# Optimization experiments

Hardware: AMD Instinct MI355X
Metric: run time of the kernel (lower is better)

The kernel has to match this reference:

```python
import jax, jax.numpy as jnp
import numpy as np

B, N_O, N_Q = 2, 512, 512
POS_DIM, LATENT, HEADS, HEAD_DIM, OUT_DIM = 3, 256, 8, 32, 128
HD = HEADS * HEAD_DIM  # == LATENT here


def _lin(key, fan_in, fan_out):
    return jax.random.normal(key, (fan_in, fan_out), jnp.float32) / np.sqrt(fan_in)


def setup_inputs() -> dict:
    key = jax.random.key(0)
    ks = jax.random.split(key, 12)
    return {
        'h_obs': jax.random.normal(ks[0], (B, N_O, LATENT), jnp.float32),
        'pos_obs': jax.random.uniform(ks[1], (B, N_O, POS_DIM), jnp.float32),
        'pos_query': jax.random.uniform(ks[2], (B, N_Q, POS_DIM), jnp.float32),
        'fw1': _lin(ks[3], LATENT, LATENT), 'fb1': jnp.zeros((LATENT,), jnp.float32),
        'fw2': _lin(ks[4], LATENT, HD), 'fb2': jnp.zeros((HD,), jnp.float32),
        'log_sigma': jnp.zeros((HEADS,), jnp.float32),
        'kw1': _lin(ks[5], POS_DIM * 3, LATENT), 'kb1': jnp.zeros((LATENT,), jnp.float32),
        'kw2': _lin(ks[6], LATENT, HEADS), 'kb2': jnp.zeros((HEADS,), jnp.float32),
        'ow': _lin(ks[7], HD, OUT_DIM), 'ob': jnp.zeros((OUT_DIM,), jnp.float32),
        'vw': _lin(ks[8], HD, OUT_DIM), 'vb': jnp.zeros((OUT_DIM,), jnp.float32),
    }


def reference(h_obs, pos_obs, pos_query, fw1, fb1, fw2, fb2, log_sigma,
              kw1, kb1, kw2, kb2, ow, ob, vw, vb):
    Bv, No, _ = h_obs.shape
    Nq = pos_query.shape[1]
    # feature net -> values [B, H, N_o, D]
    v = jax.nn.relu(h_obs @ fw1 + fb1) @ fw2 + fb2
    v = v.reshape(Bv, No, HEADS, HEAD_DIM).transpose(0, 2, 1, 3)
    # pairwise relative positions [B, Nq, No, P]
    pos_q = pos_query[:, :, None, :]
    pos_o = pos_obs[:, None, :, :]
    rel = pos_q - pos_o
    dist2 = jnp.sum(rel ** 2, axis=-1)  # [B, Nq, No]
    sigma = jnp.exp(log_sigma)[None, :, None, None]
    rbf = jnp.exp(-dist2[:, None] / (sigma ** 2 + 1e-6))  # [B, H, Nq, No]
    # kernel MLP on concatenated pairwise positions [B, Nq, No, 3P] -> [B, H, Nq, No]
    ki = jnp.concatenate([
        jnp.broadcast_to(pos_q, (Bv, Nq, No, POS_DIM)),
        jnp.broadcast_to(pos_o, (Bv, Nq, No, POS_DIM)),
        rel], axis=-1)
    delta = (jax.nn.relu(ki @ kw1 + kb1) @ kw2 + kb2).transpose(0, 3, 1, 2)
    logits = jnp.log(rbf + 1e-8) + delta
    weights = jax.nn.softmax(logits, axis=-1)  # [B, H, Nq, No]
    # weighted mean over observations
    v_mean = jnp.einsum('bhqo,bhod->bhqd', weights, v)  # [B, H, Nq, D]
    h_query = v_mean.transpose(0, 2, 1, 3).reshape(Bv, Nq, HD)
    # weighted variance: sum_o w * (v_o - v_mean)^2
    residual = v[:, :, None, :, :] - v_mean[:, :, :, None, :]  # [B, H, Nq, No, D]
    var = jnp.sum(weights[..., None] * residual ** 2, axis=3)  # [B, H, Nq, D]
    var = var.transpose(0, 2, 1, 3).reshape(Bv, Nq, HD)
    mean = h_query @ ow + ob
    var_out = jax.nn.softplus(var @ vw + vb)
    return (mean, var_out)
```

## Files before the change

### kernel.cpp

```cpp
#include <hip/hip_runtime.h>
#include <math.h>

#define NB 2
#define NO 512
#define NQ 512
#define OUT_DIM 128
#define LPAD 516

typedef __attribute__((ext_vector_type(8))) short short8;
typedef __attribute__((ext_vector_type(4))) float f32x4;
typedef float v2f __attribute__((ext_vector_type(2)));

__device__ __forceinline__ float softplus_f(float x) {
  return x > 0.0f ? x + log1pf(expf(-x)) : log1pf(expf(x));
}
__device__ __forceinline__ unsigned short bf16_rne(float f) {
  unsigned u = __float_as_uint(f);
  unsigned r = u + 0x7FFFu + ((u >> 16) & 1u);
  return (unsigned short)(r >> 16);
}
__device__ __forceinline__ float bf16_to_f32(unsigned short h) {
  return __uint_as_float(((unsigned)h) << 16);
}

#if defined(__has_builtin)
#if __has_builtin(__builtin_amdgcn_cvt_pk_bf16_f32)
#define HAS_CVT_PK_BF16 1
#endif
#endif

__device__ __forceinline__ unsigned pack_bf2(float x, float y) {
#ifdef HAS_CVT_PK_BF16
  auto r = __builtin_amdgcn_cvt_pk_bf16_f32(x, y);
  unsigned u; __builtin_memcpy(&u, &r, 4);
  return u;
#else
  unsigned ux = __float_as_uint(x);
  unsigned uy = __float_as_uint(y);
  ux = ux + 0x7FFFu + ((ux >> 16) & 1u);
  uy = uy + 0x7FFFu + ((uy >> 16) & 1u);
  return (ux >> 16) | (uy & 0xFFFF0000u);
#endif
}
__device__ __forceinline__ v2f unpk_bf2(unsigned u) {
  v2f r; r.x = __uint_as_float(u << 16); r.y = __uint_as_float(u & 0xFFFF0000u);
  return r;
}
__device__ __forceinline__ v2f splat2(float x) { v2f r; r.x = x; r.y = x; return r; }
__device__ __forceinline__ v2f fma2(v2f a, v2f b, v2f c) { return __builtin_elementwise_fma(a, b, c); }
__device__ __forceinline__ v2f max2(v2f a, v2f b) { return __builtin_elementwise_max(a, b); }

__global__ __launch_bounds__(512) void prep_kernel(
    const float* __restrict__ h_obs, const float* __restrict__ fw1,
    const float* __restrict__ fb1, const float* __restrict__ fw2,
    const float* __restrict__ fb2, const float* __restrict__ pos_obs,
    const float* __restrict__ kw1, unsigned short* __restrict__ V_bf,
    unsigned short* __restrict__ AO_bf)
{
  if (blockIdx.x < 512) {
    __shared__ float s_red[2][2][256];
    __shared__ float s_hid[2][256];
    const int n  = threadIdx.x & 255;
    const int ks = threadIdx.x >> 8;
    const int r0 = blockIdx.x * 2;
    const int k0 = ks * 128;
    float a0 = 0.f, a1 = 0.f;
    #pragma unroll 8
    for (int kk = 0; kk < 128; ++kk) {
      int k = k0 + kk;
      float w = fw1[k * 256 + n];
      a0 = fmaf(h_obs[(r0 + 0) * 256 + k], w, a0);
      a1 = fmaf(h_obs[(r0 + 1) * 256 + k], w, a1);
    }
    s_red[ks][0][n] = a0; s_red[ks][1][n] = a1;
    __syncthreads();
    if (ks == 0) {
      float bb = fb1[n];
      s_hid[0][n] = fmaxf(s_red[0][0][n] + s_red[1][0][n] + bb, 0.f);
      s_hid[1][n] = fmaxf(s_red[0][1][n] + s_red[1][1][n] + bb, 0.f);
    }
    __syncthreads();
    float c0 = 0.f, c1 = 0.f;
    #pragma unroll 8
    for (int kk = 0; kk < 128; ++kk) {
      int k = k0 + kk;
      float w = fw2[k * 256 + n];
      c0 = fmaf(s_hid[0][k], w, c0);
      c1 = fmaf(s_hid[1][k], w, c1);
    }
    __syncthreads();
    s_red[ks][0][n] = c0; s_red[ks][1][n] = c1;
    __syncthreads();
    if (ks == 0) {
      float bb = fb2[n];
      V_bf[(size_t)(r0 + 0) * 256 + n] = bf16_rne(s_red[0][0][n] + s_red[1][0][n] + bb);
      V_bf[(size_t)(r0 + 1) * 256 + n] = bf16_rne(s_red[0][1][n] + s_red[1][1][n] + bb);
    }
  } else {
    const int i     = blockIdx.x - 512;
    const int b     = i >> 8;
    const int chunk = i & 255;
    const int ol    = threadIdx.x >> 8;
    const int j     = threadIdx.x & 255;
    const int o     = chunk * 2 + ol;
    float c0 = kw1[3 * 256 + j] - kw1[6 * 256 + j];
    float c1 = kw1[4 * 256 + j] - kw1[7 * 256 + j];
    float c2 = kw1[5 * 256 + j] - kw1[8 * 256 + j];
    const float* p = pos_obs + ((size_t)(b * NO + o)) * 3;
    AO_bf[(size_t)(b * NO + o) * 256 + j] =
        bf16_rne(fmaf(p[0], c0, fmaf(p[1], c1, p[2] * c2)));
  }
}

__global__ __launch_bounds__(512, 6) void attn_fused(
    const unsigned short* __restrict__ V_bf,
    const unsigned short* __restrict__ AO_bf,
    const float* __restrict__ kw1,
    const float* __restrict__ kb1,
    const float* __restrict__ kw2,
    const float* __restrict__ kb2,
    const float* __restrict__ log_sigma,
    const float* __restrict__ pos_obs,
    const float* __restrict__ pos_query,
    const float* __restrict__ ow, const float* __restrict__ obias,
    const float* __restrict__ vw, const float* __restrict__ vbias,
    float* __restrict__ out)
{
  __shared__ float s_logits[2][8 * LPAD];
  __shared__ __align__(16) char poolA[16512];
  __shared__ __align__(16) char poolB[4096];
  __shared__ float s_sum[2][8];
  __shared__ float s_invs2[8];
  __shared__ float s_kb2v[8];

  short8* Bhi    = (short8*)poolA;
  short8* Blo    = (short8*)(poolA + 8192);
  float*  s_redC = (float*)poolA;
  float*  s_pred = (float*)poolA;
  float*  s_aq   = (float*)poolB;
  float*  s_hv   = (float*)poolB;

  const int t   = threadIdx.x;
  const int bq0 = blockIdx.x * 2;
  const int b   = bq0 >> 9;

  float pqx[2], pqy[2], pqz[2];
  #pragma unroll
  for (int q = 0; q < 2; ++q) {
    pqx[q] = pos_query[(bq0 + q) * 3 + 0];
    pqy[q] = pos_query[(bq0 + q) * 3 + 1];
    pqz[q] = pos_query[(bq0 + q) * 3 + 2];
  }
  {
    const int q = t >> 8, j = t & 255;
    float c0 = kw1[0 * 256 + j] + kw1[6 * 256 + j];
    float c1 = kw1[1 * 256 + j] + kw1[7 * 256 + j];
    float c2 = kw1[2 * 256 + j] + kw1[8 * 256 + j];
    s_aq[q * 256 + j] =
        fmaf(pqx[q], c0, fmaf(pqy[q], c1, fmaf(pqz[q], c2, kb1[j])));
  }
  {
    const int kstep = t >> 6, lane = t & 63;
    const int nh = lane & 15;
    const int kb_ = kstep * 32 + ((lane >> 4) & 3) * 8;
    short8 hi8, lo8;
    #pragma unroll
    for (int i = 0; i < 8; ++i) {
      float v = (nh < 8) ? kw2[(kb_ + i) * 8 + nh] : 0.f;
      unsigned short h = bf16_rne(v);
      hi8[i] = (short)h;
      lo8[i] = (short)bf16_rne(v - bf16_to_f32(h));
    }
    Bhi[kstep * 64 + lane] = hi8;
    Blo[kstep * 64 + lane] = lo8;
  }
  if (t < 8) {
    float s = expf(log_sigma[t]);
    s_invs2[t] = 1.0f / (s * s + 1e-6f);
    s_kb2v[t]  = kb2[t];
  }
  __syncthreads();

  {
    const int o = t;
    const float* p = pos_obs + (size_t)(b * NO + o) * 3;
    float px = p[0], py = p[1], pz = p[2];
    float d2q[2];
    #pragma unroll
    for (int q = 0; q < 2; ++q) {
      float r0 = pqx[q] - px, r1 = pqy[q] - py, r2 = pqz[q] - pz;
      d2q[q] = r0 * r0 + r1 * r1 + r2 * r2;
    }
    #pragma unroll
    for (int h = 0; h < 8; ++h) {
      float inv = s_invs2[h];
      float kbv = s_kb2v[h];
      s_logits[0][h * LPAD + o] = logf(expf(-d2q[0] * inv) + 1e-8f) + kbv;
      s_logits[1][h * LPAD + o] = logf(expf(-d2q[1] * inv) + 1e-8f) + kbv;
    }
  }

  {
    const int wave = t >> 6, lane = t & 63;
    const int quad = lane >> 4, mrow = lane & 15;
    const int tb   = wave * 4;
    f32x4 C[2][4];
    #pragma unroll
    for (int q = 0; q < 2; ++q)
      #pragma unroll
      for (int jt = 0; jt < 4; ++jt) C[q][jt] = (f32x4){0.f, 0.f, 0.f, 0.f};

    for (int kstep = 0; kstep < 8; ++kstep) {
      const int koff = kstep * 32 + quad * 8;
      const v2f* aqp0 = (const v2f*)(s_aq + koff);
      const v2f* aqp1 = (const v2f*)(s_aq + 256 + koff);
      v2f aq0[4], aq1[4];
      #pragma unroll
      for (int i = 0; i < 4; ++i) { aq0[i] = aqp0[i]; aq1[i] = aqp1[i]; }
      short8 bhi = Bhi[kstep * 64 + lane];
      short8 blo = Blo[kstep * 64 + lane];
      #pragma unroll
      for (int jt = 0; jt < 4; ++jt) {
        const int o = (tb + jt) * 16 + mrow;
        int4 u = *(const int4*)(AO_bf + ((size_t)(b * NO + o) << 8) + koff);
        v2f ao[4];
        ao[0] = unpk_bf2((unsigned)u.x); ao[1] = unpk_bf2((unsigned)u.y);
        ao[2] = unpk_bf2((unsigned)u.z); ao[3] = unpk_bf2((unsigned)u.w);
        v2f z = splat2(0.f);
        int4 af0, af1;
        {
          v2f h0 = max2(aq0[0] + ao[0], z), h1 = max2(aq0[1] + ao[1], z);
          v2f h2 = max2(aq0[2] + ao[2], z), h3 = max2(aq0[3] + ao[3], z);
          af0.x = (int)pack_bf2(h0.x, h0.y); af0.y = (int)pack_bf2(h1.x, h1.y);
          af0.z = (int)pack_bf2(h2.x, h2.y); af0.w = (int)pack_bf2(h3.x, h3.y);
        }
        {
          v2f h0 = max2(aq1[0] + ao[0], z), h1 = max2(aq1[1] + ao[1], z);
          v2f h2 = max2(aq1[2] + ao[2], z), h3 = max2(aq1[3] + ao[3], z);
          af1.x = (int)pack_bf2(h0.x, h0.y); af1.y = (int)pack_bf2(h1.x, h1.y);
          af1.z = (int)pack_bf2(h2.x, h2.y); af1.w = (int)pack_bf2(h3.x, h3.y);
        }
        short8 a0 = __builtin_bit_cast(short8, af0);
        short8 a1 = __builtin_bit_cast(short8, af1);
        C[0][jt] = __builtin_amdgcn_mfma_f32_16x16x32_bf16(a0, bhi, C[0][jt], 0, 0, 0);
        C[0][jt] = __builtin_amdgcn_mfma_f32_16x16x32_bf16(a0, blo, C[0][jt], 0, 0, 0);
        C[1][jt] = __builtin_amdgcn_mfma_f32_16x16x32_bf16(a1, bhi, C[1][jt], 0, 0, 0);
        C[1][jt] = __builtin_amdgcn_mfma_f32_16x16x32_bf16(a1, blo, C[1][jt], 0, 0, 0);
      }
    }
    __syncthreads();

    const int h = lane & 15;
    if (h < 8) {
      #pragma unroll
      for (int q = 0; q < 2; ++q)
        #pragma unroll
        for (int jt = 0; jt < 4; ++jt) {
          const int ob = (tb + jt) * 16 + quad * 4;
          #pragma unroll
          for (int r = 0; r < 4; ++r)
            s_logits[q][h * LPAD + ob + r] += C[q][jt][r];
        }
    }
  }
  __syncthreads();

  {
    const int wave = t >> 6, lane = t & 63;
    #pragma unroll
    for (int cc = 0; cc < 2; ++cc) {
      const int c = wave * 2 + cc;
      const int q = c >> 3, h = c & 7;
      float* pl = &s_logits[q][h * LPAD];
      float l[8];
      float m = -1e30f;
      #pragma unroll
      for (int k = 0; k < 8; ++k) {
        l[k] = pl[k * 64 + lane];
        m = fmaxf(m, l[k]);
      }
      #pragma unroll
      for (int off = 32; off >= 1; off >>= 1) m = fmaxf(m, __shfl_xor(m, off, 64));
      float s = 0.f;
      #pragma unroll
      for (int k = 0; k < 8; ++k) {
        float p = expf(l[k] - m);
        pl[k * 64 + lane] = p;
        s += p;
      }
      #pragma unroll
      for (int off = 32; off >= 1; off >>= 1) s += __shfl_xor(s, off, 64);
      if (lane == 0) s_sum[q][h] = s;
    }
  }
  __syncthreads();

  float q1p[8];
  {
    const int s  = t >> 6;
    const int r  = t & 63;
    const int h  = r >> 3, dg = r & 7;
    const unsigned short* vb_ = V_bf + ((size_t)(b * NO) << 8) + h * 32 + dg * 4;
    const float* P0 = &s_logits[0][h * LPAD + s * 64];
    const float* P1 = &s_logits[1][h * LPAD + s * 64];
    v2f s1a0 = splat2(0.f), s1b0 = splat2(0.f), s2a0 = splat2(0.f), s2b0 = splat2(0.f);
    v2f s1a1 = splat2(0.f), s1b1 = splat2(0.f), s2a1 = splat2(0.f), s2b1 = splat2(0.f);
    const int o0 = s * 64;
    #pragma unroll 2
    for (int oi = 0; oi < 64; oi += 4) {
      float4 pv0 = *(const float4*)&P0[oi];
      float4 pv1 = *(const float4*)&P1[oi];
      #pragma unroll
      for (int i = 0; i < 4; ++i) {
        const int o = o0 + oi + i;
        uint2 vv = *(const uint2*)(vb_ + ((size_t)o << 8));
        v2f va  = unpk_bf2(vv.x);
        v2f vb2 = unpk_bf2(vv.y);
        v2f p0 = splat2((&pv0.x)[i]), p1 = splat2((&pv1.x)[i]);
        s1a0 = fma2(p0, va, s1a0);  s1b0 = fma2(p0, vb2, s1b0);
        v2f t0a = p0 * va, t0b = p0 * vb2;
        s2a0 = fma2(t0a, va, s2a0); s2b0 = fma2(t0b, vb2, s2b0);
        s1a1 = fma2(p1, va, s1a1);  s1b1 = fma2(p1, vb2, s1b1);
        v2f t1a = p1 * va, t1b = p1 * vb2;
        s2a1 = fma2(t1a, va, s2a1); s2b1 = fma2(t1b, vb2, s2b1);
      }
    }
    s_redC[0 * LPAD + t] = s1a0.x; s_redC[1 * LPAD + t] = s1a0.y;
    s_redC[2 * LPAD + t] = s1b0.x; s_redC[3 * LPAD + t] = s1b0.y;
    s_redC[4 * LPAD + t] = s2a0.x; s_redC[5 * LPAD + t] = s2a0.y;
    s_redC[6 * LPAD + t] = s2b0.x; s_redC[7 * LPAD + t] = s2b0.y;
    q1p[0] = s1a1.x; q1p[1] = s1a1.y; q1p[2] = s1b1.x; q1p[3] = s1b1.y;
    q1p[4] = s2a1.x; q1p[5] = s2a1.y; q1p[6] = s2b1.x; q1p[7] = s2b1.y;
  }
  __syncthreads();
  if (t < 256) {
    const int hd = t, h = hd >> 5, d = hd & 31, dg = d >> 2, c = d & 3;
    float S1 = 0.f, S2 = 0.f;
    #pragma unroll
    for (int s = 0; s < 8; ++s) {
      const int idx = s * 64 + h * 8 + dg;
      S1 += s_redC[c * LPAD + idx];
      S2 += s_redC[(4 + c) * LPAD + idx];
    }
    float inv = 1.0f / s_sum[0][h];
    float m1 = S1 * inv;
    float va = fmaxf(S2 * inv - m1 * m1, 0.f);
    s_hv[0 * 256 + hd] = m1;
    s_hv[1 * 256 + hd] = va;
  }
  __syncthreads();
  {
    #pragma unroll
    for (int i = 0; i < 8; ++i) s_redC[i * LPAD + t] = q1p[i];
  }
  __syncthreads();
  if (t < 256) {
    const int hd = t, h = hd >> 5, d = hd & 31, dg = d >> 2, c = d & 3;
    float S1 = 0.f, S2 = 0.f;
    #pragma unroll
    for (int s = 0; s < 8; ++s) {
      const int idx = s * 64 + h * 8 + dg;
      S1 += s_redC[c * LPAD + idx];
      S2 += s_redC[(4 + c) * LPAD + idx];
    }
    float inv = 1.0f / s_sum[1][h];
    float m1 = S1 * inv;
    float va = fmaxf(S2 * inv - m1 * m1, 0.f);
    s_hv[2 * 256 + hd] = m1;
    s_hv[3 * 256 + hd] = va;
  }
  __syncthreads();

  {
    const int ks = t >> 8, mode = (t >> 7) & 1, n = t & 127;
    const float* W  = mode ? vw : ow;
    const float* X0 = s_hv + mode * 256;
    const float* X1 = s_hv + (2 + mode) * 256;
    float a0 = 0.f, a1 = 0.f;
    const int k0 = ks * 128;
    #pragma unroll 4
    for (int k = k0; k < k0 + 128; k += 4) {
      float4 x0 = *(const float4*)&X0[k];
      float4 x1 = *(const float4*)&X1[k];
      float w0 = W[(k + 0) * 128 + n];
      float w1 = W[(k + 1) * 128 + n];
      float w2 = W[(k + 2) * 128 + n];
      float w3 = W[(k + 3) * 128 + n];
      a0 = fmaf(x0.x, w0, a0); a1 = fmaf(x1.x, w0, a1);
      a0 = fmaf(x0.y, w1, a0); a1 = fmaf(x1.y, w1, a1);
      a0 = fmaf(x0.z, w2, a0); a1 = fmaf(x1.z, w2, a1);
      a0 = fmaf(x0.w, w3, a0); a1 = fmaf(x1.w, w3, a1);
    }
    s_pred[((ks * 2 + mode) * 2 + 0) * 128 + n] = a0;
    s_pred[((ks * 2 + mode) * 2 + 1) * 128 + n] = a1;
  }
  __syncthreads();
  {
    const int q = t >> 8, mode = (t >> 7) & 1, n = t & 127;
    float v = s_pred[((0 * 2 + mode) * 2 + q) * 128 + n]
            + s_pred[((1 * 2 + mode) * 2 + q) * 128 + n]
            + (mode ? vbias[n] : obias[n]);
    if (mode) v = softplus_f(v);
    out[(size_t)mode * (NB * NQ * OUT_DIM) + (size_t)(bq0 + q) * OUT_DIM + n] = v;
  }
}

extern "C" void kernel_launch(void* const* d_in, const int* in_sizes, int n_in,
                              void* d_out, int out_size, void* d_ws, size_t ws_size,
                              hipStream_t stream)
{
  const float* h_obs     = (const float*)d_in[0];
  const float* pos_obs   = (const float*)d_in[1];
  const float* pos_query = (const float*)d_in[2];
  const float* fw1       = (const float*)d_in[3];
  const float* fb1       = (const float*)d_in[4];
  const float* fw2       = (const float*)d_in[5];
  const float* fb2       = (const float*)d_in[6];
  const float* log_sigma = (const float*)d_in[7];
  const float* kw1       = (const float*)d_in[8];
  const float* kb1       = (const float*)d_in[9];
  const float* kw2       = (const float*)d_in[10];
  const float* kb2       = (const float*)d_in[11];
  const float* ow        = (const float*)d_in[12];
  const float* ob        = (const float*)d_in[13];
  const float* vw        = (const float*)d_in[14];
  const float* vb        = (const float*)d_in[15];

  float* out = (float*)d_out;
  unsigned short* ws = (unsigned short*)d_ws;

  unsigned short* V_bf  = ws;
  unsigned short* AO_bf = ws + 262144;

  prep_kernel<<<1024, 512, 0, stream>>>(h_obs, fw1, fb1, fw2, fb2,
                                        pos_obs, kw1, V_bf, AO_bf);
  attn_fused<<<NB * NQ / 2, 512, 0, stream>>>(V_bf, AO_bf, kw1, kb1, kw2, kb2,
                                              log_sigma, pos_obs, pos_query,
                                              ow, ob, vw, vb, out);
}
```

Before: 154.2 us.

## Process one query per block with 256 threads instead of two queries per 512-thread block

Restructures the fused attention kernel so each block handles a single query with 256 threads, launching 1024 blocks instead of 512. Shared memory per block roughly halves and register pressure per thread drops, aiming for more resident blocks and better latency hiding. The cost is giving up reuse across two queries: each AO tile and V row is now loaded and unpacked once per query rather than once per pair, and the kw2 split and output weights are reloaded per query.

New measurement: 164.6 us. 1.07x slower.

```diff
diff --git a/kernel.cpp b/kernel.cpp
--- a/kernel.cpp
+++ b/kernel.cpp
@@ -6,6 +6,7 @@
 #define NQ 512
 #define OUT_DIM 128
 #define LPAD 516
+#define RPITCH 260
 
 typedef __attribute__((ext_vector_type(8))) short short8;
 typedef __attribute__((ext_vector_type(4))) float f32x4;
@@ -112,7 +113,7 @@
   }
 }
 
-__global__ __launch_bounds__(512, 6) void attn_fused(
+__global__ __launch_bounds__(256, 4) void attn_fused(
     const unsigned short* __restrict__ V_bf,
     const unsigned short* __restrict__ AO_bf,
     const float* __restrict__ kw1,
@@ -126,53 +127,51 @@
     const float* __restrict__ vw, const float* __restrict__ vbias,
     float* __restrict__ out)
 {
-  __shared__ float s_logits[2][8 * LPAD];
-  __shared__ __align__(16) char poolA[16512];
-  __shared__ __align__(16) char poolB[4096];
-  __shared__ float s_sum[2][8];
+  __shared__ float s_logits[8 * LPAD];
+  __shared__ __align__(16) char poolA[16384];
+  __shared__ __align__(16) char poolB[2048];
+  __shared__ float s_sum[8];
   __shared__ float s_invs2[8];
   __shared__ float s_kb2v[8];
 
   short8* Bhi    = (short8*)poolA;
   short8* Blo    = (short8*)(poolA + 8192);
   float*  s_redC = (float*)poolA;
-  float*  s_pred = (float*)poolA;
   float*  s_aq   = (float*)poolB;
   float*  s_hv   = (float*)poolB;
 
-  const int t   = threadIdx.x;
-  const int bq0 = blockIdx.x * 2;
-  const int b   = bq0 >> 9;
-
-  float pqx[2], pqy[2], pqz[2];
-  #pragma unroll
-  for (int q = 0; q < 2; ++q) {
-    pqx[q] = pos_query[(bq0 + q) * 3 + 0];
-    pqy[q] = pos_query[(bq0 + q) * 3 + 1];
-    pqz[q] = pos_query[(bq0 + q) * 3 + 2];
-  }
-  {
-    const int q = t >> 8, j = t & 255;
+  const int t  = threadIdx.x;
+  const int bq = blockIdx.x;
+  const int b  = bq >> 9;
+
+  const float pqx = pos_query[bq * 3 + 0];
+  const float pqy = pos_query[bq * 3 + 1];
+  const float pqz = pos_query[bq * 3 + 2];
+  {
+    const int j = t;
     float c0 = kw1[0 * 256 + j] + kw1[6 * 256 + j];
     float c1 = kw1[1 * 256 + j] + kw1[7 * 256 + j];
     float c2 = kw1[2 * 256 + j] + kw1[8 * 256 + j];
-    s_aq[q * 256 + j] =
-        fmaf(pqx[q], c0, fmaf(pqy[q], c1, fmaf(pqz[q], c2, kb1[j])));
-  }
-  {
-    const int kstep = t >> 6, lane = t & 63;
+    s_aq[j] = fmaf(pqx, c0, fmaf(pqy, c1, fmaf(pqz, c2, kb1[j])));
+  }
+  {
+    const int lane = t & 63;
     const int nh = lane & 15;
-    const int kb_ = kstep * 32 + ((lane >> 4) & 3) * 8;
-    short8 hi8, lo8;
-    #pragma unroll
-    for (int i = 0; i < 8; ++i) {
-      float v = (nh < 8) ? kw2[(kb_ + i) * 8 + nh] : 0.f;
-      unsigned short h = bf16_rne(v);
-      hi8[i] = (short)h;
-      lo8[i] = (short)bf16_rne(v - bf16_to_f32(h));
-    }
-    Bhi[kstep * 64 + lane] = hi8;
-    Blo[kstep * 64 + lane] = lo8;
+    #pragma unroll
+    for (int kk = 0; kk < 2; ++kk) {
+      const int kstep = (t >> 6) + kk * 4;
+      const int kb_ = kstep * 32 + ((lane >> 4) & 3) * 8;
+      short8 hi8, lo8;
+      #pragma unroll
+      for (int i = 0; i < 8; ++i) {
+        float v = (nh < 8) ? kw2[(kb_ + i) * 8 + nh] : 0.f;
+        unsigned short h = bf16_rne(v);
+        hi8[i] = (short)h;
+        lo8[i] = (short)bf16_rne(v - bf16_to_f32(h));
+      }
+      Bhi[kstep * 64 + lane] = hi8;
+      Blo[kstep * 64 + lane] = lo8;
+    }
   }
   if (t < 8) {
     float s = expf(log_sigma[t]);
@@ -181,71 +180,48 @@
   }
   __syncthreads();
 
-  {
-    const int o = t;
+  #pragma unroll
+  for (int oo = 0; oo < 2; ++oo) {
+    const int o = t + oo * 256;
     const float* p = pos_obs + (size_t)(b * NO + o) * 3;
-    float px = p[0], py = p[1], pz = p[2];
-    float d2q[2];
-    #pragma unroll
-    for (int q = 0; q < 2; ++q) {
-      float r0 = pqx[q] - px, r1 = pqy[q] - py, r2 = pqz[q] - pz;
-      d2q[q] = r0 * r0 + r1 * r1 + r2 * r2;
-    }
-    #pragma unroll
-    for (int h = 0; h < 8; ++h) {
-      float inv = s_invs2[h];
-      float kbv = s_kb2v[h];
-      s_logits[0][h * LPAD + o] = logf(expf(-d2q[0] * inv) + 1e-8f) + kbv;
-      s_logits[1][h * LPAD + o] = logf(expf(-d2q[1] * inv) + 1e-8f) + kbv;
-    }
+    float r0 = pqx - p[0], r1 = pqy - p[1], r2 = pqz - p[2];
+    float d2 = r0 * r0 + r1 * r1 + r2 * r2;
+    #pragma unroll
+    for (int h = 0; h < 8; ++h)
+      s_logits[h * LPAD + o] = logf(expf(-d2 * s_invs2[h]) + 1e-8f) + s_kb2v[h];
   }
 
   {
     const int wave = t >> 6, lane = t & 63;
     const int quad = lane >> 4, mrow = lane & 15;
-    const int tb   = wave * 4;
-    f32x4 C[2][4];
-    #pragma unroll
-    for (int q = 0; q < 2; ++q)
-      #pragma unroll
-      for (int jt = 0; jt < 4; ++jt) C[q][jt] = (f32x4){0.f, 0.f, 0.f, 0.f};
+    const int tb   = wave * 8;
+    f32x4 C[8];
+    #pragma unroll
+    for (int jt = 0; jt < 8; ++jt) C[jt] = (f32x4){0.f, 0.f, 0.f, 0.f};
 
     for (int kstep = 0; kstep < 8; ++kstep) {
       const int koff = kstep * 32 + quad * 8;
-      const v2f* aqp0 = (const v2f*)(s_aq + koff);
-      const v2f* aqp1 = (const v2f*)(s_aq + 256 + koff);
-      v2f aq0[4], aq1[4];
-      #pragma unroll
-      for (int i = 0; i < 4; ++i) { aq0[i] = aqp0[i]; aq1[i] = aqp1[i]; }
+      const v2f* aqp = (const v2f*)(s_aq + koff);
+      v2f aq[4];
+      #pragma unroll
+      for (int i = 0; i < 4; ++i) aq[i] = aqp[i];
       short8 bhi = Bhi[kstep * 64 + lane];
       short8 blo = Blo[kstep * 64 + lane];
-      #pragma unroll
-      for (int jt = 0; jt < 4; ++jt) {
+      #pragma unroll 4
+      for (int jt = 0; jt < 8; ++jt) {
         const int o = (tb + jt) * 16 + mrow;
         int4 u = *(const int4*)(AO_bf + ((size_t)(b * NO + o) << 8) + koff);
-        v2f ao[4];
-        ao[0] = unpk_bf2((unsigned)u.x); ao[1] = unpk_bf2((unsigned)u.y);
-        ao[2] = unpk_bf2((unsigned)u.z); ao[3] = unpk_bf2((unsigned)u.w);
         v2f z = splat2(0.f);
-        int4 af0, af1;
-        {
-          v2f h0 = max2(aq0[0] + ao[0], z), h1 = max2(aq0[1] + ao[1], z);
-          v2f h2 = max2(aq0[2] + ao[2], z), h3 = max2(aq0[3] + ao[3], z);
-          af0.x = (int)pack_bf2(h0.x, h0.y); af0.y = (int)pack_bf2(h1.x, h1.y);
-          af0.z = (int)pack_bf2(h2.x, h2.y); af0.w = (int)pack_bf2(h3.x, h3.y);
-        }
-        {
-          v2f h0 = max2(aq1[0] + ao[0], z), h1 = max2(aq1[1] + ao[1], z);
-          v2f h2 = max2(aq1[2] + ao[2], z), h3 = max2(aq1[3] + ao[3], z);
-          af1.x = (int)pack_bf2(h0.x, h0.y); af1.y = (int)pack_bf2(h1.x, h1.y);
-          af1.z = (int)pack_bf2(h2.x, h2.y); af1.w = (int)pack_bf2(h3.x, h3.y);
-        }
-        short8 a0 = __builtin_bit_cast(short8, af0);
-        short8 a1 = __builtin_bit_cast(short8, af1);
-        C[0][jt] = __builtin_amdgcn_mfma_f32_16x16x32_bf16(a0, bhi, C[0][jt], 0, 0, 0);
-        C[0][jt] = __builtin_amdgcn_mfma_f32_16x16x32_bf16(a0, blo, C[0][jt], 0, 0, 0);
-        C[1][jt] = __builtin_amdgcn_mfma_f32_16x16x32_bf16(a1, bhi, C[1][jt], 0, 0, 0);
-        C[1][jt] = __builtin_amdgcn_mfma_f32_16x16x32_bf16(a1, blo, C[1][jt], 0, 0, 0);
+        v2f h0 = max2(aq[0] + unpk_bf2((unsigned)u.x), z);
+        v2f h1 = max2(aq[1] + unpk_bf2((unsigned)u.y), z);
+        v2f h2 = max2(aq[2] + unpk_bf2((unsigned)u.z), z);
+        v2f h3 = max2(aq[3] + unpk_bf2((unsigned)u.w), z);
+        int4 af;
+        af.x = (int)pack_bf2(h0.x, h0.y); af.y = (int)pack_bf2(h1.x, h1.y);
+        af.z = (int)pack_bf2(h2.x, h2.y); af.w = (int)pack_bf2(h3.x, h3.y);
+        short8 a = __builtin_bit_cast(short8, af);
+        C[jt] = __builtin_amdgcn_mfma_f32_16x16x32_bf16(a, bhi, C[jt], 0, 0, 0);
+        C[jt] = __builtin_amdgcn_mfma_f32_16x16x32_bf16(a, blo, C[jt], 0, 0, 0);
       }
     }
     __syncthreads();
@@ -253,14 +229,12 @@
     const int h = lane & 15;
     if (h < 8) {
       #pragma unroll
-      for (int q = 0; q < 2; ++q)
+      for (int jt = 0; jt < 8; ++jt) {
+        const int ob = (tb + jt) * 16 + quad * 4;
         #pragma unroll
-        for (int jt = 0; jt < 4; ++jt) {
-          const int ob = (tb + jt) * 16 + quad * 4;
-          #pragma unroll
-          for (int r = 0; r < 4; ++r)
-            s_logits[q][h * LPAD + ob + r] += C[q][jt][r];
-        }
+        for (int r = 0; r < 4; ++r)
+          s_logits[h * LPAD + ob + r] += C[jt][r];
+      }
     }
   }
   __syncthreads();
@@ -269,9 +243,8 @@
     const int wave = t >> 6, lane = t & 63;
     #pragma unroll
     for (int cc = 0; cc < 2; ++cc) {
-      const int c = wave * 2 + cc;
-      const int q = c >> 3, h = c & 7;
-      float* pl = &s_logits[q][h * LPAD];
+      const int h = wave * 2 + cc;
+      float* pl = &s_logits[h * LPAD];
       float l[8];
       float m = -1e30f;
       #pragma unroll
@@ -290,118 +263,75 @@
       }
       #pragma unroll
       for (int off = 32; off >= 1; off >>= 1) s += __shfl_xor(s, off, 64);
-      if (lane == 0) s_sum[q][h] = s;
-    }
-  }
-  __syncthreads();
-
-  float q1p[8];
+      if (lane == 0) s_sum[h] = s;
+    }
+  }
+  __syncthreads();
+
   {
     const int s  = t >> 6;
     const int r  = t & 63;
     const int h  = r >> 3, dg = r & 7;
     const unsigned short* vb_ = V_bf + ((size_t)(b * NO) << 8) + h * 32 + dg * 4;
-    const float* P0 = &s_logits[0][h * LPAD + s * 64];
-    const float* P1 = &s_logits[1][h * LPAD + s * 64];
-    v2f s1a0 = splat2(0.f), s1b0 = splat2(0.f), s2a0 = splat2(0.f), s2b0 = splat2(0.f);
-    v2f s1a1 = splat2(0.f), s1b1 = splat2(0.f), s2a1 = splat2(0.f), s2b1 = splat2(0.f);
-    const int o0 = s * 64;
+    const float* P = &s_logits[h * LPAD + s * 128];
+    v2f s1a = splat2(0.f), s1b = splat2(0.f), s2a = splat2(0.f), s2b = splat2(0.f);
+    const int o0 = s * 128;
     #pragma unroll 2
-    for (int oi = 0; oi < 64; oi += 4) {
-      float4 pv0 = *(const float4*)&P0[oi];
-      float4 pv1 = *(const float4*)&P1[oi];
+    for (int oi = 0; oi < 128; oi += 4) {
+      float4 pv = *(const float4*)&P[oi];
       #pragma unroll
       for (int i = 0; i < 4; ++i) {
         const int o = o0 + oi + i;
         uint2 vv = *(const uint2*)(vb_ + ((size_t)o << 8));
         v2f va  = unpk_bf2(vv.x);
         v2f vb2 = unpk_bf2(vv.y);
-        v2f p0 = splat2((&pv0.x)[i]), p1 = splat2((&pv1.x)[i]);
-        s1a0 = fma2(p0, va, s1a0);  s1b0 = fma2(p0, vb2, s1b0);
-        v2f t0a = p0 * va, t0b = p0 * vb2;
-        s2a0 = fma2(t0a, va, s2a0); s2b0 = fma2(t0b, vb2, s2b0);
-        s1a1 = fma2(p1, va, s1a1);  s1b1 = fma2(p1, vb2, s1b1);
-        v2f t1a = p1 * va, t1b = p1 * vb2;
-        s2a1 = fma2(t1a, va, s2a1); s2b1 = fma2(t1b, vb2, s2b1);
-      }
-    }
-    s_redC[0 * LPAD + t] = s1a0.x; s_redC[1 * LPAD + t] = s1a0.y;
-    s_redC[2 * LPAD + t] = s1b0.x; s_redC[3 * LPAD + t] = s1b0.y;
-    s_redC[4 * LPAD + t] = s2a0.x; s_redC[5 * LPAD + t] = s2a0.y;
-    s_redC[6 * LPAD + t] = s2b0.x; s_redC[7 * LPAD + t] = s2b0.y;
-    q1p[0] = s1a1.x; q1p[1] = s1a1.y; q1p[2] = s1b1.x; q1p[3] = s1b1.y;
-    q1p[4] = s2a1.x; q1p[5] = s2a1.y; q1p[6] = s2b1.x; q1p[7] = s2b1.y;
-  }
-  __syncthreads();
-  if (t < 256) {
+        v2f p = splat2((&pv.x)[i]);
+        s1a = fma2(p, va, s1a);  s1b = fma2(p, vb2, s1b);
+        v2f ta = p * va, tb = p * vb2;
+        s2a = fma2(ta, va, s2a); s2b = fma2(tb, vb2, s2b);
+      }
+    }
+    __syncthreads();
+    s_redC[0 * RPITCH + t] = s1a.x; s_redC[1 * RPITCH + t] = s1a.y;
+    s_redC[2 * RPITCH + t] = s1b.x; s_redC[3 * RPITCH + t] = s1b.y;
+    s_redC[4 * RPITCH + t] = s2a.x; s_redC[5 * RPITCH + t] = s2a.y;
+    s_redC[6 * RPITCH + t] = s2b.x; s_redC[7 * RPITCH + t] = s2b.y;
+  }
+  __syncthreads();
+
+  {
     const int hd = t, h = hd >> 5, d = hd & 31, dg = d >> 2, c = d & 3;
     float S1 = 0.f, S2 = 0.f;
     #pragma unroll
-    for (int s = 0; s < 8; ++s) {
+    for (int s = 0; s < 4; ++s) {
       const int idx = s * 64 + h * 8 + dg;
-      S1 += s_redC[c * LPAD + idx];
-      S2 += s_redC[(4 + c) * LPAD + idx];
-    }
-    float inv = 1.0f / s_sum[0][h];
+      S1 += s_redC[c * RPITCH + idx];
+      S2 += s_redC[(4 + c) * RPITCH + idx];
+    }
+    float inv = 1.0f / s_sum[h];
     float m1 = S1 * inv;
     float va = fmaxf(S2 * inv - m1 * m1, 0.f);
+    __syncthreads();
     s_hv[0 * 256 + hd] = m1;
     s_hv[1 * 256 + hd] = va;
   }
   __syncthreads();
-  {
-    #pragma unroll
-    for (int i = 0; i < 8; ++i) s_redC[i * LPAD + t] = q1p[i];
-  }
-  __syncthreads();
-  if (t < 256) {
-    const int hd = t, h = hd >> 5, d = hd & 31, dg = d >> 2, c = d & 3;
-    float S1 = 0.f, S2 = 0.f;
-    #pragma unroll
-    for (int s = 0; s < 8; ++s) {
-      const int idx = s * 64 + h * 8 + dg;
-      S1 += s_redC[c * LPAD + idx];
-      S2 += s_redC[(4 + c) * LPAD + idx];
-    }
-    float inv = 1.0f / s_sum[1][h];
-    float m1 = S1 * inv;
-    float va = fmaxf(S2 * inv - m1 * m1, 0.f);
-    s_hv[2 * 256 + hd] = m1;
-    s_hv[3 * 256 + hd] = va;
-  }
-  __syncthreads();
-
-  {
-    const int ks = t >> 8, mode = (t >> 7) & 1, n = t & 127;
+
+  {
+    const int mode = t >> 7, n = t & 127;
     const float* W  = mode ? vw : ow;
-    const float* X0 = s_hv + mode * 256;
-    const float* X1 = s_hv + (2 + mode) * 256;
-    float a0 = 0.f, a1 = 0.f;
-    const int k0 = ks * 128;
+    const float* X  = s_hv + mode * 256;
+    float acc = mode ? vbias[n] : obias[n];
     #pragma unroll 4
-    for (int k = k0; k < k0 + 128; k += 4) {
-      float4 x0 = *(const float4*)&X0[k];
-      float4 x1 = *(const float4*)&X1[k];
-      float w0 = W[(k + 0) * 128 + n];
-      float w1 = W[(k + 1) * 128 + n];
-      float w2 = W[(k + 2) * 128 + n];
-      float w3 = W[(k + 3) * 128 + n];
-      a0 = fmaf(x0.x, w0, a0); a1 = fmaf(x1.x, w0, a1);
-      a0 = fmaf(x0.y, w1, a0); a1 = fmaf(x1.y, w1, a1);
-      a0 = fmaf(x0.z, w2, a0); a1 = fmaf(x1.z, w2, a1);
-      a0 = fmaf(x0.w, w3, a0); a1 = fmaf(x1.w, w3, a1);
-    }
-    s_pred[((ks * 2 + mode) * 2 + 0) * 128 + n] = a0;
-    s_pred[((ks * 2 + mode) * 2 + 1) * 128 + n] = a1;
-  }
-  __syncthreads();
-  {
-    const int q = t >> 8, mode = (t >> 7) & 1, n = t & 127;
-    float v = s_pred[((0 * 2 + mode) * 2 + q) * 128 + n]
-            + s_pred[((1 * 2 + mode) * 2 + q) * 128 + n]
-            + (mode ? vbias[n] : obias[n]);
-    if (mode) v = softplus_f(v);
-    out[(size_t)mode * (NB * NQ * OUT_DIM) + (size_t)(bq0 + q) * OUT_DIM + n] = v;
+    for (int k = 0; k < 256; k += 4) {
+      float4 x = *(const float4*)&X[k];
+      acc = fmaf(x.x, W[(k + 0) * 128 + n], acc);
+      acc = fmaf(x.y, W[(k + 1) * 128 + n], acc);
+      acc = fmaf(x.z, W[(k + 2) * 128 + n], acc);
+      acc = fmaf(x.w, W[(k + 3) * 128 + n], acc);
+    }
+    if (mode) acc = softplus_f(acc);
+    out[(size_t)mode * (NB * NQ * OUT_DIM) + (size_t)bq * OUT_DIM + n] = acc;
   }
 }
 
@@ -434,7 +364,7 @@
 
   prep_kernel<<<1024, 512, 0, stream>>>(h_obs, fw1, fb1, fw2, fb2,
                                         pos_obs, kw1, V_bf, AO_bf);
-  attn_fused<<<NB * NQ / 2, 512, 0, stream>>>(V_bf, AO_bf, kw1, kb1, kw2, kb2,
-                                              log_sigma, pos_obs, pos_query,
-                                              ow, ob, vw, vb, out);
-}
+  attn_fused<<<NB * NQ, 256, 0, stream>>>(V_bf, AO_bf, kw1, kb1, kw2, kb2,
+                                          log_sigma, pos_obs, pos_query,
+                                          ow, ob, vw, vb, out);
+}
```

## Fuse RBF logits into MFMA epilogue and restructure value reduction per query

Applied to the files above, without the earlier changes.

The RBF log-term computation moves out of its separate pass: squared distances are precomputed into shared memory and the log/exp term is added in the MFMA epilogue, which removes one sync and a read-modify-write of the logits. The weighted mean/variance loop now assigns each thread one query with 8 dims via 16-byte loads instead of two queries with 4 dims. This doubles the shared reduction buffer so both queries reduce in one pass, dropping two barriers. Fast __expf/__logf intrinsics replace expf/logf/log1pf, and the occupancy hint is dropped, at some accuracy and LDS-occupancy risk.

Measured after the change: 159.8 us. 1.04x slower.

```diff
diff --git a/kernel.cpp b/kernel.cpp
--- a/kernel.cpp
+++ b/kernel.cpp
@@ -6,13 +6,14 @@
 #define NQ 512
 #define OUT_DIM 128
 #define LPAD 516
+#define RP2  516
 
 typedef __attribute__((ext_vector_type(8))) short short8;
 typedef __attribute__((ext_vector_type(4))) float f32x4;
 typedef float v2f __attribute__((ext_vector_type(2)));
 
 __device__ __forceinline__ float softplus_f(float x) {
-  return x > 0.0f ? x + log1pf(expf(-x)) : log1pf(expf(x));
+  return x > 0.0f ? x + __logf(1.0f + __expf(-x)) : __logf(1.0f + __expf(x));
 }
 __device__ __forceinline__ unsigned short bf16_rne(float f) {
   unsigned u = __float_as_uint(f);
@@ -112,7 +113,7 @@
   }
 }
 
-__global__ __launch_bounds__(512, 6) void attn_fused(
+__global__ __launch_bounds__(512) void attn_fused(
     const unsigned short* __restrict__ V_bf,
     const unsigned short* __restrict__ AO_bf,
     const float* __restrict__ kw1,
@@ -127,8 +128,8 @@
     float* __restrict__ out)
 {
   __shared__ float s_logits[2][8 * LPAD];
-  __shared__ __align__(16) char poolA[16512];
-  __shared__ __align__(16) char poolB[4096];
+  __shared__ __align__(16) char poolA[33024];
+  __shared__ __align__(16) char poolB[6144];
   __shared__ float s_sum[2][8];
   __shared__ float s_invs2[8];
   __shared__ float s_kb2v[8];
@@ -138,6 +139,7 @@
   float*  s_redC = (float*)poolA;
   float*  s_pred = (float*)poolA;
   float*  s_aq   = (float*)poolB;
+  float*  s_d2   = (float*)(poolB + 2048);
   float*  s_hv   = (float*)poolB;
 
   const int t   = threadIdx.x;
@@ -160,6 +162,16 @@
         fmaf(pqx[q], c0, fmaf(pqy[q], c1, fmaf(pqz[q], c2, kb1[j])));
   }
   {
+    const int o = t;
+    const float* p = pos_obs + (size_t)(b * NO + o) * 3;
+    float px = p[0], py = p[1], pz = p[2];
+    #pragma unroll
+    for (int q = 0; q < 2; ++q) {
+      float r0 = pqx[q] - px, r1 = pqy[q] - py, r2 = pqz[q] - pz;
+      s_d2[q * 512 + o] = r0 * r0 + r1 * r1 + r2 * r2;
+    }
+  }
+  {
     const int kstep = t >> 6, lane = t & 63;
     const int nh = lane & 15;
     const int kb_ = kstep * 32 + ((lane >> 4) & 3) * 8;
@@ -175,30 +187,11 @@
     Blo[kstep * 64 + lane] = lo8;
   }
   if (t < 8) {
-    float s = expf(log_sigma[t]);
+    float s = __expf(log_sigma[t]);
     s_invs2[t] = 1.0f / (s * s + 1e-6f);
     s_kb2v[t]  = kb2[t];
   }
   __syncthreads();
-
-  {
-    const int o = t;
-    const float* p = pos_obs + (size_t)(b * NO + o) * 3;
-    float px = p[0], py = p[1], pz = p[2];
-    float d2q[2];
-    #pragma unroll
-    for (int q = 0; q < 2; ++q) {
-      float r0 = pqx[q] - px, r1 = pqy[q] - py, r2 = pqz[q] - pz;
-      d2q[q] = r0 * r0 + r1 * r1 + r2 * r2;
-    }
-    #pragma unroll
-    for (int h = 0; h < 8; ++h) {
-      float inv = s_invs2[h];
-      float kbv = s_kb2v[h];
-      s_logits[0][h * LPAD + o] = logf(expf(-d2q[0] * inv) + 1e-8f) + kbv;
-      s_logits[1][h * LPAD + o] = logf(expf(-d2q[1] * inv) + 1e-8f) + kbv;
-    }
-  }
 
   {
     const int wave = t >> 6, lane = t & 63;
@@ -248,18 +241,22 @@
         C[1][jt] = __builtin_amdgcn_mfma_f32_16x16x32_bf16(a1, blo, C[1][jt], 0, 0, 0);
       }
     }
-    __syncthreads();
-
     const int h = lane & 15;
     if (h < 8) {
+      const float inv = s_invs2[h];
+      const float kbv = s_kb2v[h];
       #pragma unroll
       for (int q = 0; q < 2; ++q)
         #pragma unroll
         for (int jt = 0; jt < 4; ++jt) {
           const int ob = (tb + jt) * 16 + quad * 4;
           #pragma unroll
-          for (int r = 0; r < 4; ++r)
-            s_logits[q][h * LPAD + ob + r] += C[q][jt][r];
+          for (int r = 0; r < 4; ++r) {
+            const int o = ob + r;
+            float d2 = s_d2[q * 512 + o];
+            float lg = __logf(__expf(-d2 * inv) + 1e-8f) + kbv + C[q][jt][r];
+            s_logits[q][h * LPAD + o] = lg;
+          }
         }
     }
   }
@@ -284,7 +281,7 @@
       float s = 0.f;
       #pragma unroll
       for (int k = 0; k < 8; ++k) {
-        float p = expf(l[k] - m);
+        float p = __expf(l[k] - m);
         pl[k * 64 + lane] = p;
         s += p;
       }
@@ -295,79 +292,63 @@
   }
   __syncthreads();
 
-  float q1p[8];
-  {
-    const int s  = t >> 6;
-    const int r  = t & 63;
-    const int h  = r >> 3, dg = r & 7;
-    const unsigned short* vb_ = V_bf + ((size_t)(b * NO) << 8) + h * 32 + dg * 4;
-    const float* P0 = &s_logits[0][h * LPAD + s * 64];
-    const float* P1 = &s_logits[1][h * LPAD + s * 64];
-    v2f s1a0 = splat2(0.f), s1b0 = splat2(0.f), s2a0 = splat2(0.f), s2b0 = splat2(0.f);
-    v2f s1a1 = splat2(0.f), s1b1 = splat2(0.f), s2a1 = splat2(0.f), s2b1 = splat2(0.f);
+  {
+    const int q  = t >> 8;
+    const int rr = t & 255;
+    const int s  = rr >> 5;
+    const int h  = (rr >> 2) & 7;
+    const int dg = rr & 3;
+    const unsigned short* vb_ = V_bf + ((size_t)(b * NO) << 8) + h * 32 + dg * 8;
+    const float* P = &s_logits[q][h * LPAD + s * 64];
+    v2f s1[4], s2[4];
+    #pragma unroll
+    for (int i = 0; i < 4; ++i) { s1[i] = splat2(0.f); s2[i] = splat2(0.f); }
     const int o0 = s * 64;
     #pragma unroll 2
     for (int oi = 0; oi < 64; oi += 4) {
-      float4 pv0 = *(const float4*)&P0[oi];
-      float4 pv1 = *(const float4*)&P1[oi];
+      float4 pv = *(const float4*)&P[oi];
       #pragma unroll
       for (int i = 0; i < 4; ++i) {
         const int o = o0 + oi + i;
-        uint2 vv = *(const uint2*)(vb_ + ((size_t)o << 8));
-        v2f va  = unpk_bf2(vv.x);
-        v2f vb2 = unpk_bf2(vv.y);
-        v2f p0 = splat2((&pv0.x)[i]), p1 = splat2((&pv1.x)[i]);
-        s1a0 = fma2(p0, va, s1a0);  s1b0 = fma2(p0, vb2, s1b0);
-        v2f t0a = p0 * va, t0b = p0 * vb2;
-        s2a0 = fma2(t0a, va, s2a0); s2b0 = fma2(t0b, vb2, s2b0);
-        s1a1 = fma2(p1, va, s1a1);  s1b1 = fma2(p1, vb2, s1b1);
-        v2f t1a = p1 * va, t1b = p1 * vb2;
-        s2a1 = fma2(t1a, va, s2a1); s2b1 = fma2(t1b, vb2, s2b1);
+        uint4 vv = *(const uint4*)(vb_ + ((size_t)o << 8));
+        v2f p = splat2((&pv.x)[i]);
+        v2f v0 = unpk_bf2(vv.x), v1 = unpk_bf2(vv.y);
+        v2f v2 = unpk_bf2(vv.z), v3 = unpk_bf2(vv.w);
+        s1[0] = fma2(p, v0, s1[0]); s1[1] = fma2(p, v1, s1[1]);
+        s1[2] = fma2(p, v2, s1[2]); s1[3] = fma2(p, v3, s1[3]);
+        v2f t0 = p * v0, t1 = p * v1, t2 = p * v2, t3 = p * v3;
+        s2[0] = fma2(t0, v0, s2[0]); s2[1] = fma2(t1, v1, s2[1]);
+        s2[2] = fma2(t2, v2, s2[2]); s2[3] = fma2(t3, v3, s2[3]);
       }
     }
-    s_redC[0 * LPAD + t] = s1a0.x; s_redC[1 * LPAD + t] = s1a0.y;
-    s_redC[2 * LPAD + t] = s1b0.x; s_redC[3 * LPAD + t] = s1b0.y;
-    s_redC[4 * LPAD + t] = s2a0.x; s_redC[5 * LPAD + t] = s2a0.y;
-    s_redC[6 * LPAD + t] = s2b0.x; s_redC[7 * LPAD + t] = s2b0.y;
-    q1p[0] = s1a1.x; q1p[1] = s1a1.y; q1p[2] = s1b1.x; q1p[3] = s1b1.y;
-    q1p[4] = s2a1.x; q1p[5] = s2a1.y; q1p[6] = s2b1.x; q1p[7] = s2b1.y;
-  }
-  __syncthreads();
-  if (t < 256) {
-    const int hd = t, h = hd >> 5, d = hd & 31, dg = d >> 2, c = d & 3;
+    #pragma unroll
+    for (int i = 0; i < 4; ++i) {
+      s_redC[(2 * i + 0) * RP2 + t] = s1[i].x;
+      s_redC[(2 * i + 1) * RP2 + t] = s1[i].y;
+      s_redC[(8 + 2 * i + 0) * RP2 + t] = s2[i].x;
+      s_redC[(8 + 2 * i + 1) * RP2 + t] = s2[i].y;
+    }
+  }
+  __syncthreads();
+
+  {
+    const int q  = t >> 8;
+    const int hd = t & 255;
+    const int h  = hd >> 5, d = hd & 31;
+    const int dgr = d >> 3, c = d & 7;
     float S1 = 0.f, S2 = 0.f;
     #pragma unroll
     for (int s = 0; s < 8; ++s) {
-      const int idx = s * 64 + h * 8 + dg;
-      S1 += s_redC[c * LPAD + idx];
-      S2 += s_redC[(4 + c) * LPAD + idx];
-    }
-    float inv = 1.0f / s_sum[0][h];
+      const int col = q * 256 + s * 32 + h * 4 + dgr;
+      S1 += s_redC[c * RP2 + col];
+      S2 += s_redC[(8 + c) * RP2 + col];
+    }
+    float inv = 1.0f / s_sum[q][h];
     float m1 = S1 * inv;
     float va = fmaxf(S2 * inv - m1 * m1, 0.f);
-    s_hv[0 * 256 + hd] = m1;
-    s_hv[1 * 256 + hd] = va;
-  }
-  __syncthreads();
-  {
-    #pragma unroll
-    for (int i = 0; i < 8; ++i) s_redC[i * LPAD + t] = q1p[i];
-  }
-  __syncthreads();
-  if (t < 256) {
-    const int hd = t, h = hd >> 5, d = hd & 31, dg = d >> 2, c = d & 3;
-    float S1 = 0.f, S2 = 0.f;
-    #pragma unroll
-    for (int s = 0; s < 8; ++s) {
-      const int idx = s * 64 + h * 8 + dg;
-      S1 += s_redC[c * LPAD + idx];
-      S2 += s_redC[(4 + c) * LPAD + idx];
-    }
-    float inv = 1.0f / s_sum[1][h];
-    float m1 = S1 * inv;
-    float va = fmaxf(S2 * inv - m1 * m1, 0.f);
-    s_hv[2 * 256 + hd] = m1;
-    s_hv[3 * 256 + hd] = va;
+    __syncthreads();
+    s_hv[(q * 2 + 0) * 256 + hd] = m1;
+    s_hv[(q * 2 + 1) * 256 + hd] = va;
   }
   __syncthreads();
 
@@ -391,6 +372,7 @@
       a0 = fmaf(x0.z, w2, a0); a1 = fmaf(x1.z, w2, a1);
       a0 = fmaf(x0.w, w3, a0); a1 = fmaf(x1.w, w3, a1);
     }
+    __syncthreads();
     s_pred[((ks * 2 + mode) * 2 + 0) * 128 + n] = a0;
     s_pred[((ks * 2 + mode) * 2 + 1) * 128 + n] = a1;
   }
```
